# Kernel optimization log

Measured on AMD Instinct MI355X. Metric: run time of the kernel, lower is better.

The kernel has to match this reference:

```python
import jax, jax.numpy as jnp
import numpy as np

H = 256  # hidden_size
B, LQ, LK = 4, 4096, 4096


def setup_inputs() -> dict:
    key = jax.random.key(0)
    ks = jax.random.split(key, 9)
    s = 1.0 / np.sqrt(H)
    return {
        "q": jax.random.normal(ks[0], (B, LQ, H), jnp.float32),
        "k": jax.random.normal(ks[1], (B, LK, H), jnp.float32),
        "v": jax.random.normal(ks[2], (B, LK, H), jnp.float32),
        "Wq": jax.random.uniform(ks[3], (H, H), jnp.float32, -s, s),
        "bq": jax.random.uniform(ks[4], (H,), jnp.float32, -s, s),
        "Wk": jax.random.uniform(ks[5], (H, H), jnp.float32, -s, s),
        "bk": jax.random.uniform(ks[6], (H,), jnp.float32, -s, s),
        "Wv": jax.random.uniform(ks[7], (H, H), jnp.float32, -s, s),
        "bv": jax.random.uniform(ks[8], (H,), jnp.float32, -s, s),
    }


def reference(q, k, v, Wq, bq, Wk, bk, Wv, bv):
    # Linear projections (torch Linear: x @ W.T + b)
    query = jnp.einsum('bsh,oh->bso', q, Wq) + bq
    keys = jnp.einsum('bsh,oh->bso', k, Wk) + bk
    values = jnp.einsum('bsh,oh->bso', v, Wv) + bv
    scores = jnp.einsum('bqh,bkh->bqk', query, keys) / jnp.sqrt(jnp.float32(H))
    weights = jax.nn.softmax(scores, axis=-1)
    context = jnp.einsum('bqk,bkh->bqh', weights, values)
    return context
```

## Files before the change

kernel.cpp:

```cpp
#include <hip/hip_runtime.h>
#include <hip/hip_bf16.h>
#include <stdint.h>

#define HD   256
#define SEQ  4096
#define NB   4
#define NTOK (NB * SEQ)
#define NEL  ((size_t)NTOK * HD)

typedef __hip_bfloat16 bf16;
typedef short    bf16x8  __attribute__((ext_vector_type(8)));
typedef float    f32x16  __attribute__((ext_vector_type(16)));
typedef float    f32x4_t __attribute__((ext_vector_type(4)));
typedef uint32_t u32x2_t __attribute__((ext_vector_type(2)));

__device__ __forceinline__ uint32_t pk2bf(float a, float b) {
  uint32_t ua = __builtin_bit_cast(uint32_t, a);
  uint32_t ub = __builtin_bit_cast(uint32_t, b);
  return ((ua + 0x8000u) >> 16) | ((ub + 0x8000u) & 0xFFFF0000u);
}
__device__ __forceinline__ uint16_t f2bf(float a) {
  uint32_t u = __builtin_bit_cast(uint32_t, a);
  return (uint16_t)((u + 0x8000u) >> 16);
}

__global__ __launch_bounds__(256, 2) void proj_kernel(
    const float* __restrict__ Xq, const float* __restrict__ Xk, const float* __restrict__ Xv,
    const float* __restrict__ Wq, const float* __restrict__ Wk, const float* __restrict__ Wv,
    const float* __restrict__ bq, const float* __restrict__ bk, const float* __restrict__ bv,
    bf16* __restrict__ out0, float cexp) {
  const int which = (int)blockIdx.y;
  const float* X    = which == 0 ? Xq : which == 1 ? Xk : Xv;
  const float* W    = which == 0 ? Wq : which == 1 ? Wk : Wv;
  const float* bias = which == 0 ? bq : which == 1 ? bk : bv;
  bf16* out = out0 + (size_t)which * NEL;
  const float scale = which == 0 ? cexp : 1.0f;

  __shared__ bf16 xl[64][264];
  const int tid = (int)threadIdx.x;
  const int w = tid >> 6, l = tid & 63;
  const int m = l & 31, h = l >> 5;
  const int m0 = (int)blockIdx.x * 64;

#pragma unroll
  for (int j = 0; j < 16; ++j) {
    int e = j * 256 + tid;
    int row = e >> 6, c4 = e & 63;
    f32x4_t v = *(const f32x4_t*)(X + (size_t)(m0 + row) * HD + c4 * 4);
    u32x2_t pk; pk.x = pk2bf(v.x, v.y); pk.y = pk2bf(v.z, v.w);
    *(u32x2_t*)(&xl[row][c4 * 4]) = pk;
  }
  __syncthreads();

  f32x16 acc00 = {}, acc01 = {}, acc10 = {}, acc11 = {};

#pragma unroll
  for (int kh = 0; kh < 2; ++kh) {
    bf16x8 bfr[2][8];
#pragma unroll
    for (int nt2 = 0; nt2 < 2; ++nt2)
#pragma unroll
      for (int ks = 0; ks < 8; ++ks) {
        const float* wp = W + (size_t)(w * 64 + nt2 * 32 + m) * HD + (kh * 8 + ks) * 16 + h * 8;
        f32x4_t w0 = *(const f32x4_t*)wp;
        f32x4_t w1 = *(const f32x4_t*)(wp + 4);
        union { uint32_t u[4]; bf16x8 v; } cv;
        cv.u[0] = pk2bf(w0.x, w0.y); cv.u[1] = pk2bf(w0.z, w0.w);
        cv.u[2] = pk2bf(w1.x, w1.y); cv.u[3] = pk2bf(w1.z, w1.w);
        bfr[nt2][ks] = cv.v;
      }
#pragma unroll
    for (int ks = 0; ks < 8; ++ks) {
      int kbyte = (kh * 8 + ks) * 32 + h * 16;
      bf16x8 a0 = *(const bf16x8*)((const char*)&xl[m][0] + kbyte);
      bf16x8 a1 = *(const bf16x8*)((const char*)&xl[32 + m][0] + kbyte);
      acc00 = __builtin_amdgcn_mfma_f32_32x32x16_bf16(a0, bfr[0][ks], acc00, 0, 0, 0);
      acc01 = __builtin_amdgcn_mfma_f32_32x32x16_bf16(a0, bfr[1][ks], acc01, 0, 0, 0);
      acc10 = __builtin_amdgcn_mfma_f32_32x32x16_bf16(a1, bfr[0][ks], acc10, 0, 0, 0);
      acc11 = __builtin_amdgcn_mfma_f32_32x32x16_bf16(a1, bfr[1][ks], acc11, 0, 0, 0);
    }
  }
  __syncthreads();

  float bv0 = bias[w * 64 + m];
  float bv1 = bias[w * 64 + 32 + m];
#pragma unroll
  for (int r = 0; r < 16; ++r) {
    int row = (r & 3) + ((r >> 2) << 3) + 4 * h;
    xl[row][w * 64 + m]           = __builtin_bit_cast(bf16, f2bf((acc00[r] + bv0) * scale));
    xl[row][w * 64 + 32 + m]      = __builtin_bit_cast(bf16, f2bf((acc01[r] + bv1) * scale));
    xl[32 + row][w * 64 + m]      = __builtin_bit_cast(bf16, f2bf((acc10[r] + bv0) * scale));
    xl[32 + row][w * 64 + 32 + m] = __builtin_bit_cast(bf16, f2bf((acc11[r] + bv1) * scale));
  }
  __syncthreads();
#pragma unroll
  for (int j = 0; j < 8; ++j) {
    int unit = j * 256 + tid;
    int row = unit >> 5, uc = unit & 31;
    f32x4_t vv = *(const f32x4_t*)((const char*)&xl[row][0] + uc * 16);
    *(f32x4_t*)(out + (size_t)(m0 + row) * HD + uc * 8) = vv;
  }
}

__global__ __launch_bounds__(256, 2) void transpose_kernel(
    const bf16* __restrict__ Vp, bf16* __restrict__ Vt) {
  __shared__ bf16 tl[64][70];
  const int tid = (int)threadIdx.x;
  const int m0 = (int)blockIdx.x * 64, n0 = (int)blockIdx.y * 64;
  const int batch = m0 >> 12, s0 = m0 & (SEQ - 1);
#pragma unroll
  for (int j = 0; j < 4; ++j) {
    int unit = j * 256 + tid;
    int row = unit >> 4, qc = unit & 15;
    u32x2_t v = *(const u32x2_t*)(Vp + (size_t)(m0 + row) * HD + n0 + qc * 4);
    uint32_t* dst = (uint32_t*)&tl[row][qc * 4];
    dst[0] = v.x; dst[1] = v.y;
  }
  __syncthreads();
#pragma unroll
  for (int j = 0; j < 4; ++j) {
    int unit = j * 256 + tid;
    int orow = unit >> 4, oc = unit & 15;
    uint32_t w0 = (uint32_t)__builtin_bit_cast(uint16_t, tl[oc * 4 + 0][orow]) |
                  ((uint32_t)__builtin_bit_cast(uint16_t, tl[oc * 4 + 1][orow]) << 16);
    uint32_t w1 = (uint32_t)__builtin_bit_cast(uint16_t, tl[oc * 4 + 2][orow]) |
                  ((uint32_t)__builtin_bit_cast(uint16_t, tl[oc * 4 + 3][orow]) << 16);
    uint32_t* dst = (uint32_t*)(Vt + (size_t)batch * HD * SEQ + (size_t)(n0 + orow) * SEQ + s0 + oc * 4);
    dst[0] = w0; dst[1] = w1;
  }
}

__global__ __launch_bounds__(256, 2) void attn_kernel(
    const bf16* __restrict__ Qp, const bf16* __restrict__ Kp,
    const bf16* __restrict__ Vt, float* __restrict__ Op,
    float* __restrict__ Lp, int kvlen) {
  __shared__ __align__(128) char smem[65536];
  char* Kl = smem;
  char* Vl = smem + 32768;

  const int tid = (int)threadIdx.x;
  const int w = tid >> 6, l = tid & 63;
  const int m = l & 31, h = l >> 5;
  const int qt = (int)blockIdx.x, b = (int)blockIdx.y, sp = (int)blockIdx.z;
  const int kvbase = sp * kvlen;
  const int niter = kvlen >> 5;

  const int gq = b * SEQ + qt * 128 + w * 32 + m;
  bf16x8 qf[16];
#pragma unroll
  for (int ks = 0; ks < 16; ++ks)
    qf[ks] = *(const bf16x8*)(Qp + (size_t)gq * HD + ks * 16 + h * 8);

  f32x16 oacc[8] = {};
  float Lacc = 0.f;

  auto stage = [&](int buf, int kv0) {
#pragma unroll
    for (int i = 0; i < 4; ++i) {
      int kk = i * 8 + w * 2 + (l >> 5);
      int s = (l & 31) ^ (kk & 31);
      const bf16* src = Kp + (size_t)(b * SEQ + kv0 + kk) * HD + s * 8;
      __builtin_amdgcn_global_load_lds(
          (const __attribute__((address_space(1))) void*)src,
          (__attribute__((address_space(3))) void*)(Kl + buf * 16384 + i * 4096 + w * 1024),
          16, 0, 0);
    }
#pragma unroll
    for (int i = 0; i < 4; ++i) {
      int r = i * 16 + w * 4 + (l >> 4);
      int x = (l & 15) ^ (r & 15);
      int d = (r << 2) + (x >> 2), j = x & 3;
      const bf16* src = Vt + (size_t)b * HD * SEQ + (size_t)d * SEQ + kv0 + j * 8;
      __builtin_amdgcn_global_load_lds(
          (const __attribute__((address_space(1))) void*)src,
          (__attribute__((address_space(3))) void*)(Vl + buf * 16384 + i * 4096 + w * 1024),
          16, 0, 0);
    }
  };

  stage(0, kvbase);

  for (int t = 0; t < niter; ++t) {
    const int cur = t & 1;

    asm volatile("s_barrier" ::: "memory");
    if (t + 1 < niter) {
      stage(cur ^ 1, kvbase + (t + 1) * 32);
      asm volatile("s_waitcnt vmcnt(8)" ::: "memory");
    } else {
      asm volatile("s_waitcnt vmcnt(0)" ::: "memory");
    }
    asm volatile("s_barrier" ::: "memory");

    f32x16 s0 = {};
    const char* kb = Kl + cur * 16384 + m * 512;
    __builtin_amdgcn_s_setprio(1);
#pragma unroll
    for (int ks = 0; ks < 16; ++ks) {
      bf16x8 k0 = *(const bf16x8*)(kb + (((2 * ks + h) ^ m) << 4));
      s0 = __builtin_amdgcn_mfma_f32_32x32x16_bf16(k0, qf[ks], s0, 0, 0, 0);
    }
    __builtin_amdgcn_s_setprio(0);

    float p[16];
#pragma unroll
    for (int r = 0; r < 16; ++r) p[r] = __builtin_exp2f(s0[r]);
    float ls = 0.f;
#pragma unroll
    for (int r = 0; r < 16; ++r) ls += p[r];
    Lacc += ls;

    bf16x8 pf[2];
#pragma unroll
    for (int ks = 0; ks < 2; ++ks) {
      int o = ks * 8;
      uint32_t P0, P1, P2, P3;
      asm("v_cvt_pk_bf16_f32 %0, %1, %2" : "=v"(P0) : "v"(p[o + 0]), "v"(p[o + 1]));
      asm("v_cvt_pk_bf16_f32 %0, %1, %2" : "=v"(P1) : "v"(p[o + 2]), "v"(p[o + 3]));
      asm("v_cvt_pk_bf16_f32 %0, %1, %2" : "=v"(P2) : "v"(p[o + 4]), "v"(p[o + 5]));
      asm("v_cvt_pk_bf16_f32 %0, %1, %2" : "=v"(P3) : "v"(p[o + 6]), "v"(p[o + 7]));
      asm volatile("v_permlane32_swap_b32 %0, %1" : "+v"(P0), "+v"(P2));
      asm volatile("v_permlane32_swap_b32 %0, %1" : "+v"(P1), "+v"(P3));
      union { uint32_t u[4]; bf16x8 v; } cv;
      cv.u[0] = P0; cv.u[1] = P1; cv.u[2] = P2; cv.u[3] = P3;
      pf[ks] = cv.v;
    }

    const char* vb = Vl + cur * 16384;
    __builtin_amdgcn_s_setprio(1);
#pragma unroll
    for (int dt = 0; dt < 8; ++dt) {
      int d = dt * 32 + m;
      int r = d >> 2;
#pragma unroll
      for (int ks = 0; ks < 2; ++ks) {
        int x = (((d & 3) << 2) | (2 * ks + h)) ^ (r & 15);
        bf16x8 vf = *(const bf16x8*)(vb + r * 256 + x * 16);
        oacc[dt] = __builtin_amdgcn_mfma_f32_32x32x16_bf16(vf, pf[ks], oacc[dt], 0, 0, 0);
      }
    }
    __builtin_amdgcn_s_setprio(0);
  }

  float Lrow = Lacc + __shfl_xor(Lacc, 32, 64);
  if (l < 32)
    Lp[(size_t)sp * NTOK + b * SEQ + qt * 128 + w * 32 + m] = Lrow;

#pragma unroll
  for (int half = 0; half < 2; ++half) {
    __syncthreads();
    if ((w >> 1) == half) {
      const int ql = (w & 1) * 32 + m;
#pragma unroll
      for (int dt = 0; dt < 8; ++dt)
#pragma unroll
        for (int rq = 0; rq < 4; ++rq) {
          int drow = dt * 32 + rq * 8 + 4 * h;
          f32x4_t vv;
          vv.x = oacc[dt][rq * 4 + 0]; vv.y = oacc[dt][rq * 4 + 1];
          vv.z = oacc[dt][rq * 4 + 2]; vv.w = oacc[dt][rq * 4 + 3];
          int slot = (drow >> 2) ^ (ql & 31);
          *(f32x4_t*)(smem + ql * 1024 + slot * 16) = vv;
        }
    }
    __syncthreads();
#pragma unroll
    for (int j = 0; j < 16; ++j) {
      int unit = j * 256 + tid;
      int qq = unit >> 6, sl = unit & 63;
      f32x4_t vv = *(const f32x4_t*)(smem + qq * 1024 + ((sl ^ (qq & 31)) << 4));
      int gqq = b * SEQ + qt * 128 + half * 64 + qq;
      *(f32x4_t*)(Op + (size_t)sp * NEL + (size_t)gqq * HD + sl * 4) = vv;
    }
  }
}

__global__ __launch_bounds__(256, 2) void combine_kernel(
    const float* __restrict__ Op, const float* __restrict__ Lp,
    float* __restrict__ out, int nsplit) {
  size_t qd = (size_t)blockIdx.x * 256 + threadIdx.x;
  int row = (int)(qd >> 6);
  f32x4_t v = ((const f32x4_t*)Op)[qd];
  float Ls = Lp[row];
  for (int s = 1; s < nsplit; ++s) {
    f32x4_t v2 = ((const f32x4_t*)Op)[qd + (size_t)s * (NEL >> 2)];
    v.x += v2.x; v.y += v2.y; v.z += v2.z; v.w += v2.w;
    Ls += Lp[(size_t)s * NTOK + row];
  }
  float inv = 1.f / Ls;
  v.x *= inv; v.y *= inv; v.z *= inv; v.w *= inv;
  ((f32x4_t*)out)[qd] = v;
}

extern "C" void kernel_launch(void* const* d_in, const int* in_sizes, int n_in,
                              void* d_out, int out_size, void* d_ws, size_t ws_size,
                              hipStream_t stream) {
  (void)in_sizes; (void)n_in; (void)out_size;
  const float* q  = (const float*)d_in[0];
  const float* k  = (const float*)d_in[1];
  const float* v  = (const float*)d_in[2];
  const float* Wq = (const float*)d_in[3];
  const float* bq = (const float*)d_in[4];
  const float* Wk = (const float*)d_in[5];
  const float* bk = (const float*)d_in[6];
  const float* Wv = (const float*)d_in[7];
  const float* bv = (const float*)d_in[8];

  char* ws = (char*)d_ws;
  bf16* Qp = (bf16*)ws;
  bf16* Vp = Qp + 2 * NEL;
  bf16* Vt = Vp + NEL;
  bf16* Kp = Qp + NEL;
  float* Op = (float*)(ws + 4 * NEL * sizeof(bf16));

  int nsplit = 1;
  for (int cand = 4; cand > 1; cand >>= 1) {
    size_t need = 4 * NEL * sizeof(bf16) + (size_t)cand * NEL * sizeof(float) +
                  (size_t)cand * NTOK * sizeof(float);
    if (ws_size >= need) { nsplit = cand; break; }
  }
  float* Lp = Op + (size_t)nsplit * NEL;

  const float CEXP = 0.09016844f;

  proj_kernel<<<dim3(NTOK / 64, 3), 256, 0, stream>>>(q, k, v, Wq, Wk, Wv, bq, bk, bv, Qp, CEXP);
  transpose_kernel<<<dim3(NTOK / 64, HD / 64), 256, 0, stream>>>(Vp, Vt);
  attn_kernel<<<dim3(SEQ / 128, NB, nsplit), 256, 0, stream>>>(Qp, Kp, Vt, Op, Lp, SEQ / nsplit);
  combine_kernel<<<(int)((NEL / 4) / 256), 256, 0, stream>>>(Op, Lp, (float*)d_out, nsplit);
}
```

Baseline: 136.1 us.

## Software-pipeline attention loop by interleaving next QK^T with current PV MFMAs

The attention main loop is restructured so the QK^T MFMAs for tile t+1 are interleaved with the PV MFMAs for tile t. K is now prefetched two tiles ahead and V one tile ahead, using separate K and V staging. The exp/bf16 pack of the previous scores runs while the next loads are in flight. This is meant to hide the softmax latency and the serial MFMA dependency chain, at the cost of more live registers (the s0 accumulator stays live across iterations), a redundant QK computation and redundant loads on the last iteration.

```diff
diff --git a/kernel.cpp b/kernel.cpp
--- a/kernel.cpp
+++ b/kernel.cpp
@@ -154,7 +154,7 @@
   f32x16 oacc[8] = {};
   float Lacc = 0.f;
 
-  auto stage = [&](int buf, int kv0) {
+  auto stage_K = [&](int buf, int kv0) {
 #pragma unroll
     for (int i = 0; i < 4; ++i) {
       int kk = i * 8 + w * 2 + (l >> 5);
@@ -165,6 +165,8 @@
           (__attribute__((address_space(3))) void*)(Kl + buf * 16384 + i * 4096 + w * 1024),
           16, 0, 0);
     }
+  };
+  auto stage_V = [&](int buf, int kv0) {
 #pragma unroll
     for (int i = 0; i < 4; ++i) {
       int r = i * 16 + w * 4 + (l >> 4);
@@ -178,22 +180,15 @@
     }
   };
 
-  stage(0, kvbase);
-
-  for (int t = 0; t < niter; ++t) {
-    const int cur = t & 1;
-
-    asm volatile("s_barrier" ::: "memory");
-    if (t + 1 < niter) {
-      stage(cur ^ 1, kvbase + (t + 1) * 32);
-      asm volatile("s_waitcnt vmcnt(8)" ::: "memory");
-    } else {
-      asm volatile("s_waitcnt vmcnt(0)" ::: "memory");
-    }
-    asm volatile("s_barrier" ::: "memory");
-
-    f32x16 s0 = {};
-    const char* kb = Kl + cur * 16384 + m * 512;
+  stage_K(0, kvbase);
+  stage_K(1, kvbase + 32);
+  stage_V(0, kvbase);
+  asm volatile("s_waitcnt vmcnt(8)" ::: "memory");
+  asm volatile("s_barrier" ::: "memory");
+
+  f32x16 s0 = {};
+  {
+    const char* kb = Kl + m * 512;
     __builtin_amdgcn_s_setprio(1);
 #pragma unroll
     for (int ks = 0; ks < 16; ++ks) {
@@ -201,43 +196,56 @@
       s0 = __builtin_amdgcn_mfma_f32_32x32x16_bf16(k0, qf[ks], s0, 0, 0, 0);
     }
     __builtin_amdgcn_s_setprio(0);
-
-    float p[16];
-#pragma unroll
-    for (int r = 0; r < 16; ++r) p[r] = __builtin_exp2f(s0[r]);
+  }
+
+  for (int t = 0; t < niter; ++t) {
+    asm volatile("s_barrier" ::: "memory");
+    int tk = t + 2 < niter ? t + 2 : niter - 1;
+    int tv = t + 1 < niter ? t + 1 : niter - 1;
+    stage_K(t & 1, kvbase + tk * 32);
+    stage_V((t + 1) & 1, kvbase + tv * 32);
+
+    bf16x8 pf[2];
     float ls = 0.f;
 #pragma unroll
-    for (int r = 0; r < 16; ++r) ls += p[r];
-    Lacc += ls;
-
-    bf16x8 pf[2];
-#pragma unroll
-    for (int ks = 0; ks < 2; ++ks) {
-      int o = ks * 8;
+    for (int ks2 = 0; ks2 < 2; ++ks2) {
       uint32_t P0, P1, P2, P3;
-      asm("v_cvt_pk_bf16_f32 %0, %1, %2" : "=v"(P0) : "v"(p[o + 0]), "v"(p[o + 1]));
-      asm("v_cvt_pk_bf16_f32 %0, %1, %2" : "=v"(P1) : "v"(p[o + 2]), "v"(p[o + 3]));
-      asm("v_cvt_pk_bf16_f32 %0, %1, %2" : "=v"(P2) : "v"(p[o + 4]), "v"(p[o + 5]));
-      asm("v_cvt_pk_bf16_f32 %0, %1, %2" : "=v"(P3) : "v"(p[o + 6]), "v"(p[o + 7]));
+      {
+        float e0 = __builtin_exp2f(s0[ks2 * 8 + 0]), e1 = __builtin_exp2f(s0[ks2 * 8 + 1]);
+        float e2 = __builtin_exp2f(s0[ks2 * 8 + 2]), e3 = __builtin_exp2f(s0[ks2 * 8 + 3]);
+        float e4 = __builtin_exp2f(s0[ks2 * 8 + 4]), e5 = __builtin_exp2f(s0[ks2 * 8 + 5]);
+        float e6 = __builtin_exp2f(s0[ks2 * 8 + 6]), e7 = __builtin_exp2f(s0[ks2 * 8 + 7]);
+        ls += ((e0 + e1) + (e2 + e3)) + ((e4 + e5) + (e6 + e7));
+        asm("v_cvt_pk_bf16_f32 %0, %1, %2" : "=v"(P0) : "v"(e0), "v"(e1));
+        asm("v_cvt_pk_bf16_f32 %0, %1, %2" : "=v"(P1) : "v"(e2), "v"(e3));
+        asm("v_cvt_pk_bf16_f32 %0, %1, %2" : "=v"(P2) : "v"(e4), "v"(e5));
+        asm("v_cvt_pk_bf16_f32 %0, %1, %2" : "=v"(P3) : "v"(e6), "v"(e7));
+      }
       asm volatile("v_permlane32_swap_b32 %0, %1" : "+v"(P0), "+v"(P2));
       asm volatile("v_permlane32_swap_b32 %0, %1" : "+v"(P1), "+v"(P3));
       union { uint32_t u[4]; bf16x8 v; } cv;
       cv.u[0] = P0; cv.u[1] = P1; cv.u[2] = P2; cv.u[3] = P3;
-      pf[ks] = cv.v;
-    }
-
-    const char* vb = Vl + cur * 16384;
+      pf[ks2] = cv.v;
+    }
+    Lacc += ls;
+    s0 = (f32x16){};
+
+    asm volatile("s_waitcnt vmcnt(8)" ::: "memory");
+    asm volatile("s_barrier" ::: "memory");
+
+    const char* kb = Kl + (((t + 1) & 1) << 14) + m * 512;
+    const char* vb = Vl + ((t & 1) << 14);
     __builtin_amdgcn_s_setprio(1);
 #pragma unroll
-    for (int dt = 0; dt < 8; ++dt) {
+    for (int i = 0; i < 16; ++i) {
+      bf16x8 k0 = *(const bf16x8*)(kb + (((2 * i + h) ^ m) << 4));
+      s0 = __builtin_amdgcn_mfma_f32_32x32x16_bf16(k0, qf[i], s0, 0, 0, 0);
+      int dt = i >> 1, ks = i & 1;
       int d = dt * 32 + m;
       int r = d >> 2;
-#pragma unroll
-      for (int ks = 0; ks < 2; ++ks) {
-        int x = (((d & 3) << 2) | (2 * ks + h)) ^ (r & 15);
-        bf16x8 vf = *(const bf16x8*)(vb + r * 256 + x * 16);
-        oacc[dt] = __builtin_amdgcn_mfma_f32_32x32x16_bf16(vf, pf[ks], oacc[dt], 0, 0, 0);
-      }
+      int x = (((d & 3) << 2) | (2 * ks + h)) ^ (r & 15);
+      bf16x8 vf = *(const bf16x8*)(vb + r * 256 + x * 16);
+      oacc[dt] = __builtin_amdgcn_mfma_f32_32x32x16_bf16(vf, pf[ks], oacc[dt], 0, 0, 0);
     }
     __builtin_amdgcn_s_setprio(0);
   }
@@ -308,9 +316,9 @@
 
   char* ws = (char*)d_ws;
   bf16* Qp = (bf16*)ws;
+  bf16* Kp = Qp + NEL;
   bf16* Vp = Qp + 2 * NEL;
   bf16* Vt = Vp + NEL;
-  bf16* Kp = Qp + NEL;
   float* Op = (float*)(ws + 4 * NEL * sizeof(bf16));
 
   int nsplit = 1;
```

New measurement: 236.7 us. 73.8% more time.

## Fuse V transpose into projection, store bf16 partials, remap attention blocks

Applied to the files above, without the earlier changes.

The V projection now writes its output directly in transposed layout through shared memory, which removes the separate transpose kernel and its round trip of V through global memory. Split-K attention partial outputs are stored as bf16 instead of fp32, roughly halving the traffic between attention and the combine kernel; the combine kernel reads 8 bf16 values per thread. Attention block IDs are remapped so consecutive blocks are interleaved across 8 groups, likely to spread work across XCDs and improve L2 locality. The trade-off is extra rounding of unnormalized partial sums to bf16 before combining.

```diff
diff --git a/kernel.cpp b/kernel.cpp
--- a/kernel.cpp
+++ b/kernel.cpp
@@ -22,6 +22,9 @@
 __device__ __forceinline__ uint16_t f2bf(float a) {
   uint32_t u = __builtin_bit_cast(uint32_t, a);
   return (uint16_t)((u + 0x8000u) >> 16);
+}
+__device__ __forceinline__ float bf2f(short s) {
+  return __builtin_bit_cast(float, ((uint32_t)(uint16_t)s) << 16);
 }
 
 __global__ __launch_bounds__(256, 2) void proj_kernel(
@@ -33,10 +36,11 @@
   const float* X    = which == 0 ? Xq : which == 1 ? Xk : Xv;
   const float* W    = which == 0 ? Wq : which == 1 ? Wk : Wv;
   const float* bias = which == 0 ? bq : which == 1 ? bk : bv;
-  bf16* out = out0 + (size_t)which * NEL;
   const float scale = which == 0 ? cexp : 1.0f;
 
-  __shared__ bf16 xl[64][264];
+  __shared__ __align__(16) char praw[36864];
+  bf16 (*xl)[264] = (bf16(*)[264])praw;
+
   const int tid = (int)threadIdx.x;
   const int w = tid >> 6, l = tid & 63;
   const int m = l & 31, h = l >> 5;
@@ -84,56 +88,62 @@
 
   float bv0 = bias[w * 64 + m];
   float bv1 = bias[w * 64 + 32 + m];
-#pragma unroll
-  for (int r = 0; r < 16; ++r) {
-    int row = (r & 3) + ((r >> 2) << 3) + 4 * h;
-    xl[row][w * 64 + m]           = __builtin_bit_cast(bf16, f2bf((acc00[r] + bv0) * scale));
-    xl[row][w * 64 + 32 + m]      = __builtin_bit_cast(bf16, f2bf((acc01[r] + bv1) * scale));
-    xl[32 + row][w * 64 + m]      = __builtin_bit_cast(bf16, f2bf((acc10[r] + bv0) * scale));
-    xl[32 + row][w * 64 + 32 + m] = __builtin_bit_cast(bf16, f2bf((acc11[r] + bv1) * scale));
-  }
-  __syncthreads();
-#pragma unroll
-  for (int j = 0; j < 8; ++j) {
-    int unit = j * 256 + tid;
-    int row = unit >> 5, uc = unit & 31;
-    f32x4_t vv = *(const f32x4_t*)((const char*)&xl[row][0] + uc * 16);
-    *(f32x4_t*)(out + (size_t)(m0 + row) * HD + uc * 8) = vv;
-  }
-}
-
-__global__ __launch_bounds__(256, 2) void transpose_kernel(
-    const bf16* __restrict__ Vp, bf16* __restrict__ Vt) {
-  __shared__ bf16 tl[64][70];
-  const int tid = (int)threadIdx.x;
-  const int m0 = (int)blockIdx.x * 64, n0 = (int)blockIdx.y * 64;
-  const int batch = m0 >> 12, s0 = m0 & (SEQ - 1);
-#pragma unroll
-  for (int j = 0; j < 4; ++j) {
-    int unit = j * 256 + tid;
-    int row = unit >> 4, qc = unit & 15;
-    u32x2_t v = *(const u32x2_t*)(Vp + (size_t)(m0 + row) * HD + n0 + qc * 4);
-    uint32_t* dst = (uint32_t*)&tl[row][qc * 4];
-    dst[0] = v.x; dst[1] = v.y;
-  }
-  __syncthreads();
-#pragma unroll
-  for (int j = 0; j < 4; ++j) {
-    int unit = j * 256 + tid;
-    int orow = unit >> 4, oc = unit & 15;
-    uint32_t w0 = (uint32_t)__builtin_bit_cast(uint16_t, tl[oc * 4 + 0][orow]) |
-                  ((uint32_t)__builtin_bit_cast(uint16_t, tl[oc * 4 + 1][orow]) << 16);
-    uint32_t w1 = (uint32_t)__builtin_bit_cast(uint16_t, tl[oc * 4 + 2][orow]) |
-                  ((uint32_t)__builtin_bit_cast(uint16_t, tl[oc * 4 + 3][orow]) << 16);
-    uint32_t* dst = (uint32_t*)(Vt + (size_t)batch * HD * SEQ + (size_t)(n0 + orow) * SEQ + s0 + oc * 4);
-    dst[0] = w0; dst[1] = w1;
+
+  if (which == 2) {
+    bf16 (*lt)[72] = (bf16(*)[72])praw;
+    const int n0 = w * 64 + m;
+#pragma unroll
+    for (int r2 = 0; r2 < 4; ++r2) {
+      int tok = 8 * r2 + 4 * h;
+      u32x2_t v0, v1, v2, v3;
+      v0.x = pk2bf(acc00[r2 * 4 + 0] + bv0, acc00[r2 * 4 + 1] + bv0);
+      v0.y = pk2bf(acc00[r2 * 4 + 2] + bv0, acc00[r2 * 4 + 3] + bv0);
+      v1.x = pk2bf(acc01[r2 * 4 + 0] + bv1, acc01[r2 * 4 + 1] + bv1);
+      v1.y = pk2bf(acc01[r2 * 4 + 2] + bv1, acc01[r2 * 4 + 3] + bv1);
+      v2.x = pk2bf(acc10[r2 * 4 + 0] + bv0, acc10[r2 * 4 + 1] + bv0);
+      v2.y = pk2bf(acc10[r2 * 4 + 2] + bv0, acc10[r2 * 4 + 3] + bv0);
+      v3.x = pk2bf(acc11[r2 * 4 + 0] + bv1, acc11[r2 * 4 + 1] + bv1);
+      v3.y = pk2bf(acc11[r2 * 4 + 2] + bv1, acc11[r2 * 4 + 3] + bv1);
+      *(u32x2_t*)&lt[n0][tok]            = v0;
+      *(u32x2_t*)&lt[n0 + 32][tok]       = v1;
+      *(u32x2_t*)&lt[n0][32 + tok]       = v2;
+      *(u32x2_t*)&lt[n0 + 32][32 + tok]  = v3;
+    }
+    __syncthreads();
+    bf16* Vt = out0 + 2 * NEL;
+    const int batch = m0 >> 12, sg = m0 & (SEQ - 1);
+#pragma unroll
+    for (int j = 0; j < 8; ++j) {
+      int unit = j * 256 + tid;
+      int r = unit >> 3, c = unit & 7;
+      f32x4_t vv = *(const f32x4_t*)&lt[r][c * 8];
+      *(f32x4_t*)(Vt + (size_t)batch * HD * SEQ + (size_t)r * SEQ + sg + c * 8) = vv;
+    }
+  } else {
+    bf16* out = out0 + (size_t)which * NEL;
+#pragma unroll
+    for (int r = 0; r < 16; ++r) {
+      int row = (r & 3) + ((r >> 2) << 3) + 4 * h;
+      xl[row][w * 64 + m]           = __builtin_bit_cast(bf16, f2bf((acc00[r] + bv0) * scale));
+      xl[row][w * 64 + 32 + m]      = __builtin_bit_cast(bf16, f2bf((acc01[r] + bv1) * scale));
+      xl[32 + row][w * 64 + m]      = __builtin_bit_cast(bf16, f2bf((acc10[r] + bv0) * scale));
+      xl[32 + row][w * 64 + 32 + m] = __builtin_bit_cast(bf16, f2bf((acc11[r] + bv1) * scale));
+    }
+    __syncthreads();
+#pragma unroll
+    for (int j = 0; j < 8; ++j) {
+      int unit = j * 256 + tid;
+      int row = unit >> 5, uc = unit & 31;
+      f32x4_t vv = *(const f32x4_t*)((const char*)&xl[row][0] + uc * 16);
+      *(f32x4_t*)(out + (size_t)(m0 + row) * HD + uc * 8) = vv;
+    }
   }
 }
 
 __global__ __launch_bounds__(256, 2) void attn_kernel(
     const bf16* __restrict__ Qp, const bf16* __restrict__ Kp,
-    const bf16* __restrict__ Vt, float* __restrict__ Op,
-    float* __restrict__ Lp, int kvlen) {
+    const bf16* __restrict__ Vt, bf16* __restrict__ Op,
+    float* __restrict__ Lp, int kvlen, int cpx) {
   __shared__ __align__(128) char smem[65536];
   char* Kl = smem;
   char* Vl = smem + 32768;
@@ -141,7 +151,10 @@
   const int tid = (int)threadIdx.x;
   const int w = tid >> 6, l = tid & 63;
   const int m = l & 31, h = l >> 5;
-  const int qt = (int)blockIdx.x, b = (int)blockIdx.y, sp = (int)blockIdx.z;
+
+  int fid = (int)blockIdx.x + 32 * ((int)blockIdx.y + 4 * (int)blockIdx.z);
+  int nid = (fid & 7) * cpx + (fid >> 3);
+  const int qt = nid & 31, b = (nid >> 5) & 3, sp = nid >> 7;
   const int kvbase = sp * kvlen;
   const int niter = kvlen >> 5;
 
@@ -269,27 +282,32 @@
       int unit = j * 256 + tid;
       int qq = unit >> 6, sl = unit & 63;
       f32x4_t vv = *(const f32x4_t*)(smem + qq * 1024 + ((sl ^ (qq & 31)) << 4));
+      u32x2_t pk; pk.x = pk2bf(vv.x, vv.y); pk.y = pk2bf(vv.z, vv.w);
       int gqq = b * SEQ + qt * 128 + half * 64 + qq;
-      *(f32x4_t*)(Op + (size_t)sp * NEL + (size_t)gqq * HD + sl * 4) = vv;
+      *(u32x2_t*)(Op + (size_t)sp * NEL + (size_t)gqq * HD + sl * 4) = pk;
     }
   }
 }
 
 __global__ __launch_bounds__(256, 2) void combine_kernel(
-    const float* __restrict__ Op, const float* __restrict__ Lp,
+    const bf16* __restrict__ Op, const float* __restrict__ Lp,
     float* __restrict__ out, int nsplit) {
-  size_t qd = (size_t)blockIdx.x * 256 + threadIdx.x;
-  int row = (int)(qd >> 6);
-  f32x4_t v = ((const f32x4_t*)Op)[qd];
-  float Ls = Lp[row];
-  for (int s = 1; s < nsplit; ++s) {
-    f32x4_t v2 = ((const f32x4_t*)Op)[qd + (size_t)s * (NEL >> 2)];
-    v.x += v2.x; v.y += v2.y; v.z += v2.z; v.w += v2.w;
+  size_t u = (size_t)blockIdx.x * 256 + threadIdx.x;
+  int row = (int)(u >> 5);
+  float a[8] = {};
+  float Ls = 0.f;
+  for (int s = 0; s < nsplit; ++s) {
+    bf16x8 pv = ((const bf16x8*)Op)[u + (size_t)s * (NEL >> 3)];
+#pragma unroll
+    for (int i = 0; i < 8; ++i) a[i] += bf2f(pv[i]);
     Ls += Lp[(size_t)s * NTOK + row];
   }
   float inv = 1.f / Ls;
-  v.x *= inv; v.y *= inv; v.z *= inv; v.w *= inv;
-  ((f32x4_t*)out)[qd] = v;
+  f32x4_t lo, hi;
+  lo.x = a[0] * inv; lo.y = a[1] * inv; lo.z = a[2] * inv; lo.w = a[3] * inv;
+  hi.x = a[4] * inv; hi.y = a[5] * inv; hi.z = a[6] * inv; hi.w = a[7] * inv;
+  ((f32x4_t*)out)[2 * u]     = lo;
+  ((f32x4_t*)out)[2 * u + 1] = hi;
 }
 
 extern "C" void kernel_launch(void* const* d_in, const int* in_sizes, int n_in,
@@ -307,24 +325,22 @@
   const float* bv = (const float*)d_in[8];
 
   char* ws = (char*)d_ws;
-  bf16* Qp = (bf16*)ws;
-  bf16* Vp = Qp + 2 * NEL;
-  bf16* Vt = Vp + NEL;
-  bf16* Kp = Qp + NEL;
-  float* Op = (float*)(ws + 4 * NEL * sizeof(bf16));
+  bf16* Qp  = (bf16*)ws;
+  bf16* Kp  = Qp + NEL;
+  bf16* Vt  = Qp + 2 * NEL;
+  bf16* Opb = Qp + 3 * NEL;
 
   int nsplit = 1;
   for (int cand = 4; cand > 1; cand >>= 1) {
-    size_t need = 4 * NEL * sizeof(bf16) + (size_t)cand * NEL * sizeof(float) +
-                  (size_t)cand * NTOK * sizeof(float);
+    size_t need = 3 * NEL * 2 + (size_t)cand * NEL * 2 + (size_t)cand * NTOK * 4;
     if (ws_size >= need) { nsplit = cand; break; }
   }
-  float* Lp = Op + (size_t)nsplit * NEL;
+  float* Lp = (float*)(Opb + (size_t)nsplit * NEL);
 
   const float CEXP = 0.09016844f;
 
   proj_kernel<<<dim3(NTOK / 64, 3), 256, 0, stream>>>(q, k, v, Wq, Wk, Wv, bq, bk, bv, Qp, CEXP);
-  transpose_kernel<<<dim3(NTOK / 64, HD / 64), 256, 0, stream>>>(Vp, Vt);
-  attn_kernel<<<dim3(SEQ / 128, NB, nsplit), 256, 0, stream>>>(Qp, Kp, Vt, Op, Lp, SEQ / nsplit);
-  combine_kernel<<<(int)((NEL / 4) / 256), 256, 0, stream>>>(Op, Lp, (float*)d_out, nsplit);
-}
+  attn_kernel<<<dim3(SEQ / 128, NB, nsplit), 256, 0, stream>>>(
+      Qp, Kp, Vt, Opb, Lp, SEQ / nsplit, 16 * nsplit);
+  combine_kernel<<<(int)(NEL / 8 / 256), 256, 0, stream>>>(Opb, Lp, (float*)d_out, nsplit);
+}
```

New measurement: 126.6 us. -7.0%, faster.
